# Performance work log

Measured on AMD Instinct MI355X. Metric: run time of the kernel, lower is better.

Reference implementation:

```python
import jax, jax.numpy as jnp
import numpy as np

H_OUT, W_OUT = 7, 7

def _pool_matrix(n_in, n_out):
    # M[o, i] = 1/window_size if i in [floor(o*n_in/n_out), ceil((o+1)*n_in/n_out)) else 0
    M = np.zeros((n_out, n_in), dtype=np.float32)
    for o in range(n_out):
        s = int(np.floor(o * n_in / n_out))
        e = int(np.ceil((o + 1) * n_in / n_out))
        M[o, s:e] = 1.0 / (e - s)
    return jnp.asarray(M)

def setup_inputs() -> dict:
    key = jax.random.key(0)
    x = jax.random.normal(key, (16, 768, 64, 48), dtype=jnp.float32)
    return {"x": x}

def reference(x) -> jnp.ndarray:
    H_in, W_in = x.shape[-2:]
    Mh = _pool_matrix(H_in, H_OUT).astype(x.dtype)  # [H_out, H_in]
    Mw = _pool_matrix(W_in, W_OUT).astype(x.dtype)  # [W_out, W_in]
    # adaptive avg pool as two small contractions: [B,C,H,W] -> [B,C,H,p] -> [B,C,o,p]
    t = jnp.einsum('bchw,pw->bchp', x, Mw)
    out = jnp.einsum('oh,bchp->bcop', Mh, t)
    return out
```

## Files before the change

### kernel.cpp

```cpp
#include <hip/hip_runtime.h>


#define H_IN 64
#define W_IN 48
#define HO 7
#define WO 7
#define PLANE (H_IN * W_IN)

__global__ __launch_bounds__(256) void
adaptive_pool_kernel(const float* __restrict__ x, float* __restrict__ out) {
    __shared__ float xs[PLANE];
    __shared__ float ts[H_IN * WO];

    const int plane = blockIdx.x;
    const int tid   = threadIdx.x;
    const float* xp = x + (size_t)plane * PLANE;

    const float4* xp4 = reinterpret_cast<const float4*>(xp);
    float4* xs4 = reinterpret_cast<float4*>(xs);
    #pragma unroll
    for (int i = 0; i < 3; ++i) {
        const int idx = tid + i * 256;
        xs4[idx] = xp4[idx];
    }
    __syncthreads();

    #pragma unroll
    for (int i = 0; i < 2; ++i) {
        const int item = tid + i * 256;
        if (item < H_IN * WO) {
            const int row = item / WO;
            const int ow  = item % WO;
            const int ws  = (ow * W_IN) / WO;
            const int we  = ((ow + 1) * W_IN + WO - 1) / WO;
            float s = 0.0f;
            #pragma unroll
            for (int w = 0; w < 8; ++w) {
                if (ws + w < we) s += xs[row * W_IN + ws + w];
            }
            ts[item] = s * (1.0f / (float)(we - ws));
        }
    }
    __syncthreads();

    if (tid < HO * WO) {
        const int oh = tid / WO;
        const int ow = tid % WO;
        const int hs = (oh * H_IN) / HO;
        const int he = ((oh + 1) * H_IN + HO - 1) / HO;
        float s = 0.0f;
        #pragma unroll
        for (int h = 0; h < 10; ++h) {
            if (hs + h < he) s += ts[(hs + h) * WO + ow];
        }
        out[(size_t)plane * (HO * WO) + tid] = s * (1.0f / (float)(he - hs));
    }
}

extern "C" void kernel_launch(void* const* d_in, const int* in_sizes, int n_in,
                              void* d_out, int out_size, void* d_ws, size_t ws_size,
                              hipStream_t stream) {
    const float* x = (const float*)d_in[0];
    float* out = (float*)d_out;
    const int nplanes = in_sizes[0] / PLANE;
    adaptive_pool_kernel<<<nplanes, 256, 0, stream>>>(x, out);
}
```

Baseline: 28.27 us.

## Map one wavefront per plane, pool rows in registers, use wave barriers

Each 64-lane wavefront now handles one whole plane, and each lane loads one 48-float row into registers with float4 loads. The width pooling is done entirely in registers with compile-time window bounds. Only the 64x7 intermediate goes through shared memory, synchronized with a wave barrier instead of block-wide __syncthreads, and the block packs four planes. This removes the full-plane LDS staging and block synchronization, but each lane's reads are strided by a row, which may hurt coalescing, and register use goes up.

```diff
diff --git a/kernel.cpp b/kernel.cpp
--- a/kernel.cpp
+++ b/kernel.cpp
@@ -6,54 +6,54 @@
 #define HO 7
 #define WO 7
 #define PLANE (H_IN * W_IN)
+#define WPB 4
 
 __global__ __launch_bounds__(256) void
 adaptive_pool_kernel(const float* __restrict__ x, float* __restrict__ out) {
-    __shared__ float xs[PLANE];
-    __shared__ float ts[H_IN * WO];
+    __shared__ float ts[WPB][H_IN][8];
 
-    const int plane = blockIdx.x;
-    const int tid   = threadIdx.x;
-    const float* xp = x + (size_t)plane * PLANE;
+    const int tid  = threadIdx.x;
+    const int wid  = tid >> 6;
+    const int lane = tid & 63;
+    const size_t plane = (size_t)blockIdx.x * WPB + wid;
 
-    const float4* xp4 = reinterpret_cast<const float4*>(xp);
-    float4* xs4 = reinterpret_cast<float4*>(xs);
+    const float4* rp = reinterpret_cast<const float4*>(x + plane * PLANE + lane * W_IN);
+    float4 v[12];
     #pragma unroll
-    for (int i = 0; i < 3; ++i) {
-        const int idx = tid + i * 256;
-        xs4[idx] = xp4[idx];
+    for (int k = 0; k < 12; ++k) v[k] = rp[k];
+
+    float c[W_IN];
+    #pragma unroll
+    for (int k = 0; k < 12; ++k) {
+        c[4*k+0] = v[k].x; c[4*k+1] = v[k].y; c[4*k+2] = v[k].z; c[4*k+3] = v[k].w;
     }
-    __syncthreads();
 
+    const int   WS[WO]  = {0, 6, 13, 20, 27, 34, 41};
+    const int   WE[WO]  = {7, 14, 21, 28, 35, 42, 48};
+    float w[WO];
     #pragma unroll
-    for (int i = 0; i < 2; ++i) {
-        const int item = tid + i * 256;
-        if (item < H_IN * WO) {
-            const int row = item / WO;
-            const int ow  = item % WO;
-            const int ws  = (ow * W_IN) / WO;
-            const int we  = ((ow + 1) * W_IN + WO - 1) / WO;
-            float s = 0.0f;
-            #pragma unroll
-            for (int w = 0; w < 8; ++w) {
-                if (ws + w < we) s += xs[row * W_IN + ws + w];
-            }
-            ts[item] = s * (1.0f / (float)(we - ws));
-        }
-    }
-    __syncthreads();
-
-    if (tid < HO * WO) {
-        const int oh = tid / WO;
-        const int ow = tid % WO;
-        const int hs = (oh * H_IN) / HO;
-        const int he = ((oh + 1) * H_IN + HO - 1) / HO;
+    for (int o = 0; o < WO; ++o) {
         float s = 0.0f;
         #pragma unroll
-        for (int h = 0; h < 10; ++h) {
-            if (hs + h < he) s += ts[(hs + h) * WO + ow];
-        }
-        out[(size_t)plane * (HO * WO) + tid] = s * (1.0f / (float)(he - hs));
+        for (int j = WS[o]; j < WE[o]; ++j) s += c[j];
+        w[o] = s * (1.0f / (float)(WE[o] - WS[o]));
+    }
+
+    *reinterpret_cast<float4*>(&ts[wid][lane][0]) = make_float4(w[0], w[1], w[2], w[3]);
+    *reinterpret_cast<float2*>(&ts[wid][lane][4]) = make_float2(w[4], w[5]);
+    ts[wid][lane][6] = w[6];
+
+    asm volatile("s_waitcnt lgkmcnt(0)" ::: "memory");
+    __builtin_amdgcn_wave_barrier();
+
+    if (lane < HO * WO) {
+        const int oh = lane / WO;
+        const int ow = lane % WO;
+        const int hs = (oh * H_IN) / HO;
+        float s = 0.0f;
+        #pragma unroll
+        for (int h = 0; h < 10; ++h) s += ts[wid][hs + h][ow];
+        out[plane * (HO * WO) + lane] = s * 0.1f;
     }
 }
 
@@ -63,5 +63,6 @@
     const float* x = (const float*)d_in[0];
     float* out = (float*)d_out;
     const int nplanes = in_sizes[0] / PLANE;
-    adaptive_pool_kernel<<<nplanes, 256, 0, stream>>>(x, out);
+    const int nblocks = nplanes / WPB;
+    adaptive_pool_kernel<<<nblocks, 256, 0, stream>>>(x, out);
 }
```

Measured after the change: 28.23 us. No clear change (-0.1%).
